# Kernel tuning notes

Measured on AMD Instinct MI355X. Metric: run time of the kernel, lower is better.

## Reference

```python
import jax, jax.numpy as jnp
import numpy as np

N_NODES = 100000
N_EDGES = 1600000
IN_DIM = 257
HID = 128
HEADS = 4
CH = HID // HEADS  # 32 per-head channels
EDGE_DIM = 8
N_GRAPHS = 64
NUM_CLASSES = 2
NEG_SLOPE = 0.2


def setup_inputs() -> dict:
    key = jax.random.key(0)
    ks = jax.random.split(key, 16)
    inp = {}
    inp['x'] = jax.random.normal(ks[0], (N_NODES, IN_DIM), dtype=jnp.float32)
    inp['edge_index'] = jax.random.randint(ks[1], (2, N_EDGES), 0, N_NODES, dtype=jnp.int64)
    inp['edge_attr'] = jax.random.normal(ks[2], (N_EDGES, EDGE_DIM), dtype=jnp.float32)
    inp['batch'] = jnp.sort(jax.random.randint(ks[3], (N_NODES,), 0, N_GRAPHS, dtype=jnp.int64))
    s = 0.05
    # GATConv layer 1 params
    inp['W1'] = jax.random.normal(ks[4], (IN_DIM, HID), dtype=jnp.float32) * s
    inp['att_src1'] = jax.random.normal(ks[5], (HEADS, CH), dtype=jnp.float32) * s
    inp['att_dst1'] = jax.random.normal(ks[6], (HEADS, CH), dtype=jnp.float32) * s
    inp['We1'] = jax.random.normal(ks[7], (EDGE_DIM, HID), dtype=jnp.float32) * s
    inp['att_edge1'] = jax.random.normal(ks[8], (HEADS, CH), dtype=jnp.float32) * s
    inp['b1'] = jnp.zeros((HID,), dtype=jnp.float32)
    # GATConv layer 2 params
    inp['W2'] = jax.random.normal(ks[9], (HID, HID), dtype=jnp.float32) * s
    inp['att_src2'] = jax.random.normal(ks[10], (HEADS, CH), dtype=jnp.float32) * s
    inp['att_dst2'] = jax.random.normal(ks[11], (HEADS, CH), dtype=jnp.float32) * s
    inp['We2'] = jax.random.normal(ks[12], (EDGE_DIM, HID), dtype=jnp.float32) * s
    inp['att_edge2'] = jax.random.normal(ks[13], (HEADS, CH), dtype=jnp.float32) * s
    inp['b2'] = jnp.zeros((HID,), dtype=jnp.float32)
    # classifier
    inp['Wc1'] = jax.random.normal(ks[14], (HID, 64), dtype=jnp.float32) * s
    inp['bc1'] = jnp.zeros((64,), dtype=jnp.float32)
    inp['Wc2'] = jax.random.normal(ks[15], (64, NUM_CLASSES), dtype=jnp.float32) * s
    inp['bc2'] = jnp.zeros((NUM_CLASSES,), dtype=jnp.float32)
    return inp


def gat_layer(x, src, dst, edge_attr, W, att_src, att_dst, We, att_edge, bias):
    N = x.shape[0]
    xs = (x @ W).reshape(N, HEADS, CH)                      # [N,H,C]
    a_src = jnp.sum(xs * att_src, axis=-1)                  # [N,H]
    a_dst = jnp.sum(xs * att_dst, axis=-1)                  # [N,H]
    e_proj = (edge_attr @ We).reshape(-1, HEADS, CH)        # [E,H,C]
    a_edge = jnp.sum(e_proj * att_edge, axis=-1)            # [E,H]
    alpha = a_src[src] + a_dst[dst] + a_edge                # [E,H]
    alpha = jax.nn.leaky_relu(alpha, NEG_SLOPE)
    # segment softmax over incoming edges per dst node
    amax = jax.ops.segment_max(alpha, dst, num_segments=N)
    alpha = jnp.exp(alpha - amax[dst])
    denom = jax.ops.segment_sum(alpha, dst, num_segments=N)
    alpha = alpha / (denom[dst] + 1e-16)
    msg = xs[src] * alpha[..., None]                        # [E,H,C]
    out = jax.ops.segment_sum(msg, dst, num_segments=N)     # [N,H,C]
    return out.reshape(N, HID) + bias


def reference(x, edge_index, edge_attr, batch,
              W1, att_src1, att_dst1, We1, att_edge1, b1,
              W2, att_src2, att_dst2, We2, att_edge2, b2,
              Wc1, bc1, Wc2, bc2):
    src, dst = edge_index[0], edge_index[1]
    h = jax.nn.relu(gat_layer(x, src, dst, edge_attr, W1, att_src1, att_dst1, We1, att_edge1, b1))
    # dropout layers act as identity in eval mode
    h = jax.nn.relu(gat_layer(h, src, dst, edge_attr, W2, att_src2, att_dst2, We2, att_edge2, b2))
    # global mean pool per graph
    sums = jax.ops.segment_sum(h, batch, num_segments=N_GRAPHS)
    counts = jax.ops.segment_sum(jnp.ones((h.shape[0],), h.dtype), batch, num_segments=N_GRAPHS)
    pooled = sums / jnp.maximum(counts, 1.0)[:, None]       # [G,HID]
    z = jax.nn.relu(pooled @ Wc1 + bc1)
    return z @ Wc2 + bc2                                    # [G,num_classes]
```

## Files before the change

### kernel.cpp

```cpp
#include <hip/hip_runtime.h>
#include <hip/hip_fp16.h>

#define NN 100000
#define NE 1600000
#define HID 128
#define HEADS 4
#define CH 32
#define IN_DIM 257
#define CHK 64
#define KP1 288
#define KP2 128

typedef float f32x4 __attribute__((ext_vector_type(4)));
typedef _Float16 h8 __attribute__((ext_vector_type(8)));
typedef unsigned u4v __attribute__((ext_vector_type(4)));

__device__ __forceinline__ __half2 u2h2(unsigned u) {
    union { unsigned u; __half2 h; } cv;
    cv.u = u;
    return cv.h;
}

template <bool XHALF>
__global__ __launch_bounds__(256, 4) void mfma_proj(const void* __restrict__ Xin,
                                                    const __half* __restrict__ wt16,
                                                    const float* __restrict__ att_src,
                                                    const float* __restrict__ att_dst,
                                                    __half* __restrict__ XSH,
                                                    float* __restrict__ asrc,
                                                    float* __restrict__ adst,
                                                    int K, int KP, long long maxx) {
    __shared__ __half xt[2][64][40];
    __shared__ __half wtile[2][128][40];
    int tid = threadIdx.x;
    int lane = tid & 63;
    int wv = tid >> 6;
    int block0 = blockIdx.x * 64;
    int nchunk = (K + 31) >> 5;

    int sn = tid >> 2;
    int skb = (tid & 3) * 8;
    int wn = tid >> 1;
    int woff = (tid & 1) * 16;

    f32x4 acc[8];
#pragma unroll
    for (int i = 0; i < 8; ++i) acc[i] = (f32x4){0.f, 0.f, 0.f, 0.f};

    float xr[8];
    uint4 xrh;
    uint4 wr0, wr1;

    auto loadX = [&](int k0) {
        if (XHALF) {
            const __half* Xh = (const __half*)Xin;
            long long a = (long long)(block0 + sn) * K + k0 + skb;
            if (a > maxx - 7) a = maxx - 7;
            xrh = *(const uint4*)&Xh[a];
        } else {
            const float* Xf = (const float*)Xin;
#pragma unroll
            for (int j = 0; j < 8; ++j) {
                long long a = (long long)(block0 + sn) * K + k0 + skb + j;
                if (a > maxx) a = maxx;
                xr[j] = Xf[a];
            }
        }
    };
    auto writeX = [&](int buf) {
        if (XHALF) {
            *(uint4*)&xt[buf][sn][skb] = xrh;
        } else {
            __half2 p0 = __floats2half2_rn(xr[0], xr[1]);
            __half2 p1 = __floats2half2_rn(xr[2], xr[3]);
            __half2 p2 = __floats2half2_rn(xr[4], xr[5]);
            __half2 p3 = __floats2half2_rn(xr[6], xr[7]);
            uint4 w;
            w.x = *(unsigned*)&p0; w.y = *(unsigned*)&p1;
            w.z = *(unsigned*)&p2; w.w = *(unsigned*)&p3;
            *(uint4*)&xt[buf][sn][skb] = w;
        }
    };
    auto loadW = [&](int k0) {
        const __half* src = &wt16[(long long)wn * KP + k0 + woff];
        wr0 = *(const uint4*)src;
        wr1 = *(const uint4*)(src + 8);
    };
    auto writeW = [&](int buf) {
        *(uint4*)&wtile[buf][wn][woff] = wr0;
        *(uint4*)&wtile[buf][wn][woff + 8] = wr1;
    };

    loadX(0);
    loadW(0);
    asm volatile("s_waitcnt vmcnt(0)" ::: "memory");
    writeX(0);
    writeW(0);
    __syncthreads();

    int m0 = wv * 16;
    int li = lane & 15;
    int kg = (lane >> 4) * 8;

    for (int c = 0; c < nchunk; ++c) {
        int cur = c & 1;
        bool more = (c + 1 < nchunk);
        if (more) { loadX((c + 1) * 32); loadW((c + 1) * 32); }
        uint4 av = *(const uint4*)&xt[cur][m0 + li][kg];
        h8 a = *(h8*)&av;
#pragma unroll
        for (int nt = 0; nt < 8; ++nt) {
            uint4 bv = *(const uint4*)&wtile[cur][nt * 16 + li][kg];
            h8 b = *(h8*)&bv;
            acc[nt] = __builtin_amdgcn_mfma_f32_16x16x32_f16(a, b, acc[nt], 0, 0, 0);
        }
        if (more) {
            asm volatile("s_waitcnt vmcnt(0)" ::: "memory");
            writeX(cur ^ 1);
            writeW(cur ^ 1);
        }
        __syncthreads();
    }

    float as_[8], ad_[8];
#pragma unroll
    for (int nt = 0; nt < 8; ++nt) {
        as_[nt] = att_src[nt * 16 + li];
        ad_[nt] = att_dst[nt * 16 + li];
    }
    int rbase = (lane >> 4) * 4;
#pragma unroll
    for (int r = 0; r < 4; ++r) {
        int node = block0 + m0 + rbase + r;
        bool ok = node < NN;
        if (ok) {
#pragma unroll
            for (int nt = 0; nt < 8; ++nt)
                XSH[(size_t)node * HID + nt * 16 + li] = __float2half(acc[nt][r]);
        }
#pragma unroll
        for (int h = 0; h < 4; ++h) {
            float s = acc[2 * h][r] * as_[2 * h] + acc[2 * h + 1][r] * as_[2 * h + 1];
            float d = acc[2 * h][r] * ad_[2 * h] + acc[2 * h + 1][r] * ad_[2 * h + 1];
            s += __shfl_xor(s, 1); d += __shfl_xor(d, 1);
            s += __shfl_xor(s, 2); d += __shfl_xor(d, 2);
            s += __shfl_xor(s, 4); d += __shfl_xor(d, 4);
            s += __shfl_xor(s, 8); d += __shfl_xor(d, 8);
            if (ok && li == 0) {
                asrc[node * 4 + h] = s;
                adst[node * 4 + h] = d;
            }
        }
    }
}

__global__ __launch_bounds__(256) void w_prep(const float* __restrict__ W1,
                                              const float* __restrict__ W2,
                                              __half* __restrict__ wt1,
                                              __half* __restrict__ wt2) {
    int i = blockIdx.x * 256 + threadIdx.x;
    const int tot1 = HID * KP1;
    const int tot2 = HID * KP2;
    if (i < tot1) {
        int n = i / KP1, k = i % KP1;
        wt1[i] = (k < IN_DIM) ? __float2half(W1[(size_t)k * HID + n]) : __float2half(0.f);
    } else if (i < tot1 + tot2) {
        int i2 = i - tot1;
        int n = i2 >> 7, k = i2 & 127;
        wt2[i2] = __float2half(W2[(size_t)k * HID + n]);
    }
}

__global__ void compute_ve2(const float* __restrict__ We1,
                            const float* __restrict__ ae1,
                            const float* __restrict__ We2,
                            const float* __restrict__ ae2,
                            float* __restrict__ ve1,
                            float* __restrict__ ve2) {
    int i = threadIdx.x;
    if (i >= 64) return;
    const float* We = (i < 32) ? We1 : We2;
    const float* ae = (i < 32) ? ae1 : ae2;
    float* ve = (i < 32) ? ve1 : ve2;
    int j = i & 31;
    int d = j >> 2, h = j & 3;
    float s = 0.f;
    for (int c = 0; c < CH; ++c) s += We[d * HID + h * CH + c] * ae[h * CH + c];
    ve[j] = s;
}

__global__ __launch_bounds__(256) void k_deg(const int* __restrict__ ei, int* __restrict__ deg) {
    int e = blockIdx.x * 256 + threadIdx.x;
    if (e < NE) atomicAdd(&deg[ei[NE + e]], 1);
}

__global__ __launch_bounds__(256) void scan_local(const int* __restrict__ deg,
                                                  int* __restrict__ startv,
                                                  int* __restrict__ bsum) {
    __shared__ int sh[256];
    int t = threadIdx.x;
    int base = blockIdx.x * 1024 + t * 4;
    int v0 = 0, v1 = 0, v2 = 0, v3 = 0;
    if (base + 0 < NN) v0 = deg[base + 0];
    if (base + 1 < NN) v1 = deg[base + 1];
    if (base + 2 < NN) v2 = deg[base + 2];
    if (base + 3 < NN) v3 = deg[base + 3];
    int s1 = v0 + v1, s2 = s1 + v2, s3 = s2 + v3;
    sh[t] = s3;
    __syncthreads();
    for (int off = 1; off < 256; off <<= 1) {
        int x = (t >= off) ? sh[t - off] : 0;
        __syncthreads();
        sh[t] += x;
        __syncthreads();
    }
    int thOff = sh[t] - s3;
    if (base + 0 < NN) startv[base + 0] = thOff;
    if (base + 1 < NN) startv[base + 1] = thOff + v0;
    if (base + 2 < NN) startv[base + 2] = thOff + s1;
    if (base + 3 < NN) startv[base + 3] = thOff + s2;
    if (t == 255) bsum[blockIdx.x] = sh[255];
}

__global__ __launch_bounds__(256) void scan_bsum(int* __restrict__ bsum, int nb) {
    __shared__ int sh[256];
    int t = threadIdx.x;
    int v = (t < nb) ? bsum[t] : 0;
    sh[t] = v;
    __syncthreads();
    for (int off = 1; off < 256; off <<= 1) {
        int x = (t >= off) ? sh[t - off] : 0;
        __syncthreads();
        sh[t] += x;
        __syncthreads();
    }
    if (t < nb) bsum[t] = sh[t] - v;
}

__global__ __launch_bounds__(256) void scan_add(int* __restrict__ startv,
                                                const int* __restrict__ bsum) {
    int i = blockIdx.x * 256 + threadIdx.x;
    if (i < NN) startv[i] += bsum[i >> 10];
}

__global__ __launch_bounds__(256) void k_scatter(const int* __restrict__ ei,
                                                 const int* __restrict__ startv,
                                                 int* __restrict__ cursor,
                                                 const float* __restrict__ eattr,
                                                 const float* __restrict__ ve1,
                                                 const float* __restrict__ ve2,
                                                 unsigned* __restrict__ rec) {
    __shared__ float v1[32], v2[32];
    if (threadIdx.x < 32) v1[threadIdx.x] = ve1[threadIdx.x];
    else if (threadIdx.x < 64) v2[threadIdx.x - 32] = ve2[threadIdx.x - 32];
    __syncthreads();
    int e = blockIdx.x * 256 + threadIdx.x;
    if (e >= NE) return;
    int d = ei[NE + e];
    int src = ei[e];
    float4 e0 = *(const float4*)&eattr[(size_t)e * 8];
    float4 e1 = *(const float4*)&eattr[(size_t)e * 8 + 4];
    float eav[8] = {e0.x, e0.y, e0.z, e0.w, e1.x, e1.y, e1.z, e1.w};
    float a1[4], a2[4];
#pragma unroll
    for (int hh = 0; hh < 4; ++hh) {
        float s1 = 0.f, s2 = 0.f;
#pragma unroll
        for (int dd = 0; dd < 8; ++dd) {
            s1 += eav[dd] * v1[dd * 4 + hh];
            s2 += eav[dd] * v2[dd * 4 + hh];
        }
        a1[hh] = s1;
        a2[hh] = s2;
    }
    __half2 a1lo = __floats2half2_rn(a1[0], a1[1]);
    __half2 a1hi = __floats2half2_rn(a1[2], a1[3]);
    __half2 a2lo = __floats2half2_rn(a2[0], a2[1]);
    __half2 a2hi = __floats2half2_rn(a2[2], a2[3]);
    int pos = startv[d] + atomicAdd(&cursor[d], 1);
    uint4 r0, r1;
    r0.x = (unsigned)src; r0.y = *(unsigned*)&a1lo; r0.z = *(unsigned*)&a1hi; r0.w = 0;
    r1.x = (unsigned)src; r1.y = *(unsigned*)&a2lo; r1.z = *(unsigned*)&a2hi; r1.w = 0;
    *(uint4*)&rec[(size_t)pos * 8] = r0;
    *(uint4*)&rec[(size_t)pos * 8 + 4] = r1;
}

__global__ __launch_bounds__(256) void gat_gather(const int* __restrict__ startv,
                                                  const int* __restrict__ deg,
                                                  const unsigned* __restrict__ recL,
                                                  const float* __restrict__ asrc,
                                                  const float* __restrict__ adst,
                                                  const __half* __restrict__ XSH,
                                                  const float* __restrict__ bias,
                                                  __half* __restrict__ OUT) {
    __shared__ float s_p[4][CHK * 4];
    __shared__ int s_src[4][CHK];
    int w = threadIdx.x >> 6;
    int wid = blockIdx.x * 4 + w;
    if (wid >= NN) return;
    int lane = threadIdx.x & 63;
    int s0 = startv[wid];
    int dg = deg[wid];
    float4 ad4 = *(const float4*)&adst[wid * 4];
    int h = lane >> 4;
    int c0 = lane * 2;

    float denom = 0.f, acc0 = 0.f, acc1 = 0.f;

    for (int cb = 0; cb < dg; cb += CHK) {
        int cnt = min(CHK, dg - cb);
        for (int i = lane; i < cnt; i += 64) {
            int pos = s0 + cb + i;
            u4v rv = __builtin_nontemporal_load((const u4v*)&recL[(size_t)pos * 8]);
            int s = (int)rv.x;
            s_src[w][i] = s;
            float2 ae01 = __half22float2(u2h2(rv.y));
            float2 ae23 = __half22float2(u2h2(rv.z));
            float4 as4 = *(const float4*)&asrc[s * 4];
            float a0 = as4.x + ad4.x + ae01.x;
            float a1 = as4.y + ad4.y + ae01.y;
            float a2 = as4.z + ad4.z + ae23.x;
            float a3 = as4.w + ad4.w + ae23.y;
            a0 = (a0 > 0.f) ? a0 : 0.2f * a0;
            a1 = (a1 > 0.f) ? a1 : 0.2f * a1;
            a2 = (a2 > 0.f) ? a2 : 0.2f * a2;
            a3 = (a3 > 0.f) ? a3 : 0.2f * a3;
            *(float4*)&s_p[w][i * 4] =
                make_float4(__expf(a0), __expf(a1), __expf(a2), __expf(a3));
        }
        int j = 0;
        for (; j + 7 < cnt; j += 8) {
            int sv[8];
            float pv[8];
            __half2 xv[8];
#pragma unroll
            for (int q = 0; q < 8; ++q) {
                sv[q] = s_src[w][j + q];
                pv[q] = s_p[w][(j + q) * 4 + h];
            }
#pragma unroll
            for (int q = 0; q < 8; ++q) xv[q] = *(const __half2*)&XSH[(size_t)sv[q] * HID + c0];
#pragma unroll
            for (int q = 0; q < 8; ++q) {
                float2 xf = __half22float2(xv[q]);
                denom += pv[q];
                acc0 += pv[q] * xf.x;
                acc1 += pv[q] * xf.y;
            }
        }
        for (; j < cnt; ++j) {
            int s = s_src[w][j];
            float p = s_p[w][j * 4 + h];
            float2 xf = __half22float2(*(const __half2*)&XSH[(size_t)s * HID + c0]);
            denom += p;
            acc0 += p * xf.x;
            acc1 += p * xf.y;
        }
    }
    float inv_ = 1.f / (denom + 1e-16f);
    float2 bv = *(const float2*)&bias[c0];
    float o0 = fmaxf(acc0 * inv_ + bv.x, 0.f);
    float o1 = fmaxf(acc1 * inv_ + bv.y, 0.f);
    *(__half2*)&OUT[(size_t)wid * HID + c0] = __floats2half2_rn(o0, o1);
}

#define POOL_NODES 128
__global__ __launch_bounds__(256) void pool_kernel(const __half* __restrict__ H,
                                                   const int* __restrict__ batch,
                                                   float* __restrict__ pooled,
                                                   float* __restrict__ counts) {
    int tid = threadIdx.x;
    int lane = tid & 63;
    int wvi = tid >> 6;
    int c2 = lane * 2;
    int n0 = blockIdx.x * POOL_NODES;
    int nend = min(n0 + POOL_NODES, NN);
    float a0 = 0.f, a1 = 0.f, cnt = 0.f;
    int gcur = -1;
    for (int n = n0 + wvi; n < nend; n += 4) {
        int g = batch[n];
        if (g != gcur) {
            if (gcur >= 0) {
                atomicAdd(&pooled[gcur * HID + c2], a0);
                atomicAdd(&pooled[gcur * HID + c2 + 1], a1);
                if (lane == 0) atomicAdd(&counts[gcur], cnt);
            }
            gcur = g;
            a0 = a1 = cnt = 0.f;
        }
        float2 hv = __half22float2(*(const __half2*)&H[(size_t)n * HID + c2]);
        a0 += hv.x;
        a1 += hv.y;
        cnt += 1.f;
    }
    if (gcur >= 0) {
        atomicAdd(&pooled[gcur * HID + c2], a0);
        atomicAdd(&pooled[gcur * HID + c2 + 1], a1);
        if (lane == 0) atomicAdd(&counts[gcur], cnt);
    }
}

__global__ __launch_bounds__(64) void classifier(const float* __restrict__ pooled,
                                                 const float* __restrict__ counts,
                                                 const float* __restrict__ Wc1,
                                                 const float* __restrict__ bc1,
                                                 const float* __restrict__ Wc2,
                                                 const float* __restrict__ bc2,
                                                 float* __restrict__ out) {
    __shared__ float pl[HID];
    __shared__ float z[64];
    int g = blockIdx.x, t = threadIdx.x;
    float inv = 1.f / fmaxf(counts[g], 1.f);
    pl[t] = pooled[g * HID + t] * inv;
    pl[t + 64] = pooled[g * HID + 64 + t] * inv;
    __syncthreads();
    float a = bc1[t];
    for (int k = 0; k < HID; ++k) a += pl[k] * Wc1[k * 64 + t];
    z[t] = fmaxf(a, 0.f);
    __syncthreads();
    if (t < 2) {
        float o = bc2[t];
        for (int j = 0; j < 64; ++j) o += z[j] * Wc2[j * 2 + t];
        out[g * 2 + t] = o;
    }
}

extern "C" void kernel_launch(void* const* d_in, const int* in_sizes, int n_in,
                              void* d_out, int out_size, void* d_ws, size_t ws_size,
                              hipStream_t stream) {
    const float* x = (const float*)d_in[0];
    const int* ei = (const int*)d_in[1];
    const float* eattr = (const float*)d_in[2];
    const int* batch = (const int*)d_in[3];
    const float* W1 = (const float*)d_in[4];
    const float* att_src1 = (const float*)d_in[5];
    const float* att_dst1 = (const float*)d_in[6];
    const float* We1 = (const float*)d_in[7];
    const float* att_edge1 = (const float*)d_in[8];
    const float* b1 = (const float*)d_in[9];
    const float* W2 = (const float*)d_in[10];
    const float* att_src2 = (const float*)d_in[11];
    const float* att_dst2 = (const float*)d_in[12];
    const float* We2 = (const float*)d_in[13];
    const float* att_edge2 = (const float*)d_in[14];
    const float* b2 = (const float*)d_in[15];
    const float* Wc1 = (const float*)d_in[16];
    const float* bc1 = (const float*)d_in[17];
    const float* Wc2 = (const float*)d_in[18];
    const float* bc2 = (const float*)d_in[19];
    float* out = (float*)d_out;

    __half* XSH = (__half*)d_ws;
    __half* H16 = XSH + (size_t)NN * HID;
    float* asrc = (float*)(H16 + (size_t)NN * HID);
    float* adst = asrc + (size_t)NN * 4;
    float* ve1 = adst + (size_t)NN * 4;
    float* ve2 = ve1 + 32;
    float* pooled = ve2 + 32;
    float* counts = pooled + 64 * HID;
    unsigned* rec = (unsigned*)(counts + 64);
    __half* wt1 = (__half*)(rec + (size_t)NE * 8);
    __half* wt2 = wt1 + HID * KP1;
    int* deg = (int*)(wt2 + HID * KP2);
    int* cursor = deg + NN;
    int* startv = cursor + NN;
    int* bsum = startv + NN;

    int gProj = (NN + 63) / 64;
    int gE = (NE + 255) / 256;
    int gGat = (NN + 3) / 4;
    int nScanBlk = (NN + 1023) / 1024;
    int gWP = (HID * KP1 + HID * KP2 + 255) / 256;

    hipMemsetAsync(deg, 0, (size_t)2 * NN * sizeof(int), stream);
    compute_ve2<<<1, 64, 0, stream>>>(We1, att_edge1, We2, att_edge2, ve1, ve2);
    w_prep<<<gWP, 256, 0, stream>>>(W1, W2, wt1, wt2);
    k_deg<<<gE, 256, 0, stream>>>(ei, deg);
    scan_local<<<nScanBlk, 256, 0, stream>>>(deg, startv, bsum);
    scan_bsum<<<1, 256, 0, stream>>>(bsum, nScanBlk);
    scan_add<<<(NN + 255) / 256, 256, 0, stream>>>(startv, bsum);
    k_scatter<<<gE, 256, 0, stream>>>(ei, startv, cursor, eattr, ve1, ve2, rec);

    mfma_proj<false><<<gProj, 256, 0, stream>>>(x, wt1, att_src1, att_dst1, XSH, asrc, adst,
                                                IN_DIM, KP1, (long long)NN * IN_DIM - 1);
    gat_gather<<<gGat, 256, 0, stream>>>(startv, deg, rec, asrc, adst,
                                         XSH, b1, H16);

    mfma_proj<true><<<gProj, 256, 0, stream>>>(H16, wt2, att_src2, att_dst2, XSH, asrc, adst,
                                               HID, KP2, (long long)NN * HID - 1);
    gat_gather<<<gGat, 256, 0, stream>>>(startv, deg, rec + 4, asrc, adst,
                                         XSH, b2, H16);

    hipMemsetAsync(pooled, 0, (64 * HID + 64) * sizeof(float), stream);
    pool_kernel<<<(NN + POOL_NODES - 1) / POOL_NODES, 256, 0, stream>>>(H16, batch, pooled, counts);
    classifier<<<64, 64, 0, stream>>>(pooled, counts, Wc1, bc1, Wc2, bc2, out);
}
```

Measured before the change: 442.3 us.

## Split edge scatter into coarse bucket binning then per-bucket local scatter

The single random scatter of edge records into CSR order is replaced by two passes. The first bins edges into 512-node buckets in a staging buffer. The second has one block per bucket place each edge at its final slot, so writes land in a small, cache-resident region instead of being spread across the whole record array. This trades an extra full read and write of the staged records (about 51 MB each) for better write locality and fewer contended cache lines, and it needs a second record-sized workspace buffer.

```diff
diff --git a/kernel.cpp b/kernel.cpp
--- a/kernel.cpp
+++ b/kernel.cpp
@@ -10,6 +10,8 @@
 #define CHK 64
 #define KP1 288
 #define KP2 128
+#define BSH 9
+#define NBUCK ((NN + 511) / 512)
 
 typedef float f32x4 __attribute__((ext_vector_type(4)));
 typedef _Float16 h8 __attribute__((ext_vector_type(8)));
@@ -243,13 +245,13 @@
     if (i < NN) startv[i] += bsum[i >> 10];
 }
 
-__global__ __launch_bounds__(256) void k_scatter(const int* __restrict__ ei,
-                                                 const int* __restrict__ startv,
-                                                 int* __restrict__ cursor,
-                                                 const float* __restrict__ eattr,
-                                                 const float* __restrict__ ve1,
-                                                 const float* __restrict__ ve2,
-                                                 unsigned* __restrict__ rec) {
+__global__ __launch_bounds__(256) void k_binA(const int* __restrict__ ei,
+                                              const int* __restrict__ startv,
+                                              int* __restrict__ bcur,
+                                              const float* __restrict__ eattr,
+                                              const float* __restrict__ ve1,
+                                              const float* __restrict__ ve2,
+                                              unsigned* __restrict__ stg) {
     __shared__ float v1[32], v2[32];
     if (threadIdx.x < 32) v1[threadIdx.x] = ve1[threadIdx.x];
     else if (threadIdx.x < 64) v2[threadIdx.x - 32] = ve2[threadIdx.x - 32];
@@ -277,12 +279,37 @@
     __half2 a1hi = __floats2half2_rn(a1[2], a1[3]);
     __half2 a2lo = __floats2half2_rn(a2[0], a2[1]);
     __half2 a2hi = __floats2half2_rn(a2[2], a2[3]);
-    int pos = startv[d] + atomicAdd(&cursor[d], 1);
-    uint4 r0, r1;
-    r0.x = (unsigned)src; r0.y = *(unsigned*)&a1lo; r0.z = *(unsigned*)&a1hi; r0.w = 0;
-    r1.x = (unsigned)src; r1.y = *(unsigned*)&a2lo; r1.z = *(unsigned*)&a2hi; r1.w = 0;
-    *(uint4*)&rec[(size_t)pos * 8] = r0;
-    *(uint4*)&rec[(size_t)pos * 8 + 4] = r1;
+    int b = d >> BSH;
+    int sp = startv[b << BSH] + atomicAdd(&bcur[b], 1);
+    uint4 s0, s1;
+    s0.x = (unsigned)src; s0.y = (unsigned)d;
+    s0.z = *(unsigned*)&a1lo; s0.w = *(unsigned*)&a1hi;
+    s1.x = *(unsigned*)&a2lo; s1.y = *(unsigned*)&a2hi; s1.z = 0; s1.w = 0;
+    *(uint4*)&stg[(size_t)sp * 8] = s0;
+    *(uint4*)&stg[(size_t)sp * 8 + 4] = s1;
+}
+
+__global__ __launch_bounds__(256) void k_binB(const unsigned* __restrict__ stg,
+                                              const int* __restrict__ startv,
+                                              int* __restrict__ cursor,
+                                              unsigned* __restrict__ rec) {
+    int b = blockIdx.x;
+    int nstart = b << BSH;
+    int nnext = nstart + (1 << BSH);
+    int base = startv[nstart];
+    int end = (nnext >= NN) ? NE : startv[nnext];
+    for (int p = base + threadIdx.x; p < end; p += 256) {
+        u4v s0 = __builtin_nontemporal_load((const u4v*)&stg[(size_t)p * 8]);
+        u4v s1 = __builtin_nontemporal_load((const u4v*)&stg[(size_t)p * 8 + 4]);
+        int src = (int)s0.x;
+        int d = (int)s0.y;
+        int pos = startv[d] + atomicAdd(&cursor[d], 1);
+        uint4 r0, r1;
+        r0.x = (unsigned)src; r0.y = s0.z; r0.z = s0.w; r0.w = 0;
+        r1.x = (unsigned)src; r1.y = s1.x; r1.z = s1.y; r1.w = 0;
+        *(uint4*)&rec[(size_t)pos * 8] = r0;
+        *(uint4*)&rec[(size_t)pos * 8 + 4] = r1;
+    }
 }
 
 __global__ __launch_bounds__(256) void gat_gather(const int* __restrict__ startv,
@@ -459,11 +486,13 @@
     float* pooled = ve2 + 32;
     float* counts = pooled + 64 * HID;
     unsigned* rec = (unsigned*)(counts + 64);
-    __half* wt1 = (__half*)(rec + (size_t)NE * 8);
+    unsigned* stg = rec + (size_t)NE * 8;
+    __half* wt1 = (__half*)(stg + (size_t)NE * 8);
     __half* wt2 = wt1 + HID * KP1;
     int* deg = (int*)(wt2 + HID * KP2);
     int* cursor = deg + NN;
-    int* startv = cursor + NN;
+    int* bcur = cursor + NN;
+    int* startv = bcur + 256;
     int* bsum = startv + NN;
 
     int gProj = (NN + 63) / 64;
@@ -472,14 +501,15 @@
     int nScanBlk = (NN + 1023) / 1024;
     int gWP = (HID * KP1 + HID * KP2 + 255) / 256;
 
-    hipMemsetAsync(deg, 0, (size_t)2 * NN * sizeof(int), stream);
+    hipMemsetAsync(deg, 0, ((size_t)2 * NN + 256) * sizeof(int), stream);
     compute_ve2<<<1, 64, 0, stream>>>(We1, att_edge1, We2, att_edge2, ve1, ve2);
     w_prep<<<gWP, 256, 0, stream>>>(W1, W2, wt1, wt2);
     k_deg<<<gE, 256, 0, stream>>>(ei, deg);
     scan_local<<<nScanBlk, 256, 0, stream>>>(deg, startv, bsum);
     scan_bsum<<<1, 256, 0, stream>>>(bsum, nScanBlk);
     scan_add<<<(NN + 255) / 256, 256, 0, stream>>>(startv, bsum);
-    k_scatter<<<gE, 256, 0, stream>>>(ei, startv, cursor, eattr, ve1, ve2, rec);
+    k_binA<<<gE, 256, 0, stream>>>(ei, startv, bcur, eattr, ve1, ve2, stg);
+    k_binB<<<NBUCK, 256, 0, stream>>>(stg, startv, cursor, rec);
 
     mfma_proj<false><<<gProj, 256, 0, stream>>>(x, wt1, att_src1, att_dst1, XSH, asrc, adst,
                                                 IN_DIM, KP1, (long long)NN * IN_DIM - 1);
```

Measured after the change: 1.329 ms. 3.01x slower.
